# Optimization experiments

Measured on AMD Instinct MI355X. Metric: run time of the kernel, lower is better.

## Reference

```python
import jax, jax.numpy as jnp
import numpy as np

N, E, EMB, HID, FT, H = 2000, 32000, 768, 384, 768, 4
NEG_SLOPE = 0.2


def gat_conv(x, src, dst, edge_attr, W, a_src, a_dst, W_e, a_e, b):
    """PyG GATConv, concat=False (mean over heads), edge_dim, add_self_loops
    with fill_value='mean'. x:[N,Fin], edge_attr:[E,768]."""
    n = x.shape[0]
    h, c = a_src.shape
    # self loops: edge_attr of loop (i,i) = mean of incoming edge_attr at i
    deg = jax.ops.segment_sum(jnp.ones(src.shape[0], x.dtype), dst, num_segments=n)
    loop_attr = jax.ops.segment_sum(edge_attr, dst, num_segments=n) / jnp.maximum(deg, 1.0)[:, None]
    ar = jnp.arange(n)
    s = jnp.concatenate([src, ar])
    d = jnp.concatenate([dst, ar])
    ea = jnp.concatenate([edge_attr, loop_attr], axis=0)   # [E+N, 768]
    hx = (x @ W).reshape(n, h, c)                           # [N,H,C]
    he = (ea @ W_e).reshape(-1, h, c)                       # [E+N,H,C]
    alpha = (jnp.einsum('nhc,hc->nh', hx, a_src)[s]
             + jnp.einsum('nhc,hc->nh', hx, a_dst)[d]
             + jnp.einsum('ehc,hc->eh', he, a_e))           # [E+N,H]
    alpha = jax.nn.leaky_relu(alpha, NEG_SLOPE)
    # segment softmax over destination node (self loop guarantees nonempty)
    mx = jax.ops.segment_max(alpha, d, num_segments=n)
    ex = jnp.exp(alpha - mx[d])
    den = jax.ops.segment_sum(ex, d, num_segments=n)
    att = ex / den[d]                                       # [E+N,H]
    out = jax.ops.segment_sum(hx[s] * att[:, :, None], d, num_segments=n)  # [N,H,C]
    return out.mean(axis=1) + b


def setup_inputs() -> dict:
    key = jax.random.key(0)
    ks = jax.random.split(key, 16)
    w = lambda k, shape, s=0.05: (jax.random.normal(k, shape, jnp.float32) * s)
    return {
        'x': jax.random.randint(ks[0], (N, 2), 0, 178),
        'edge_index': jax.random.randint(ks[1], (2, E), 0, N),
        'edge_attr': jax.random.randint(ks[2], (E, 2), 0, 18),
        'x_emb': w(ks[3], (178, EMB)),
        'e_emb': w(ks[4], (18, EMB)),
        'W1': w(ks[5], (EMB, H * HID)),
        'as1': w(ks[6], (H, HID)),
        'ad1': w(ks[7], (H, HID)),
        'We1': w(ks[8], (EMB, H * HID)),
        'ae1': w(ks[9], (H, HID)),
        'b1': jnp.zeros((HID,), jnp.float32),
        'W2': w(ks[10], (HID, H * FT)),
        'as2': w(ks[11], (H, FT)),
        'ad2': w(ks[12], (H, FT)),
        'We2': w(ks[13], (EMB, H * FT)),
        'ae2': w(ks[14], (H, FT)),
        'b2': jnp.zeros((FT,), jnp.float32),
    }


def reference(x, edge_index, edge_attr, x_emb, e_emb, W1, as1, ad1, We1, ae1, b1,
              W2, as2, ad2, We2, ae2, b2):
    src, dst = edge_index[0], edge_index[1]
    xf = x_emb[x].sum(axis=1)          # [N,768]
    eaf = e_emb[edge_attr].sum(axis=1)  # [E,768]
    h = jax.nn.relu(gat_conv(xf, src, dst, eaf, W1, as1, ad1, We1, ae1, b1))
    out = gat_conv(h, src, dst, eaf, W2, as2, ad2, We2, ae2, b2)
    return out
```

## Files before the change

### kernel.cpp

```cpp
#include <hip/hip_runtime.h>
#include <hip/hip_bf16.h>

#define NN   2000
#define NE   32000
#define EMBD 768
#define NH   4
#define HID  384
#define NEG  0.2f
#define DCAP 128

#define GM 2000
#define GN 768
#define GK 1536
#define K1 768

typedef __bf16 bf16x8 __attribute__((ext_vector_type(8)));
typedef float  f32x4  __attribute__((ext_vector_type(4)));

__device__ inline float wsum(float v){
#pragma unroll
  for (int o = 32; o > 0; o >>= 1) v += __shfl_xor(v, o, 64);
  return v;
}
__device__ inline float wmax(float v){
#pragma unroll
  for (int o = 32; o > 0; o >>= 1) v = fmaxf(v, __shfl_xor(v, o, 64));
  return v;
}

__device__ inline unsigned short f2bf(float f){
  unsigned u = __float_as_uint(f);
  unsigned r = (u + 0x7FFFu + ((u >> 16) & 1u)) >> 16;
  return (unsigned short)r;
}
__device__ inline float bf2f(unsigned short h){
  return __uint_as_float(((unsigned)h) << 16);
}

__device__ inline void gload16(const void* g, void* l){
  __builtin_amdgcn_global_load_lds((const __attribute__((address_space(1))) void*)g,
                                   (__attribute__((address_space(3))) void*)l, 16, 0, 0);
}
__device__ inline float dot4(float4 a, float4 b){
  return a.x*b.x + a.y*b.y + a.z*b.z + a.w*b.w;
}

__global__ __launch_bounds__(1024) void k_cnt(const int* __restrict__ dst,
                                              int* __restrict__ offsets,
                                              int* __restrict__ cursor){
  __shared__ int cnt[NN];
  __shared__ int s[1024];
  int t = threadIdx.x;
  for (int i = t; i < NN; i += 1024) cnt[i] = 0;
  __syncthreads();
  for (int e = t; e < NE; e += 1024) atomicAdd(&cnt[dst[e]], 1);
  __syncthreads();
  int a = (2*t   < NN) ? cnt[2*t  ] : 0;
  int b = (2*t+1 < NN) ? cnt[2*t+1] : 0;
  s[t] = a + b;
  __syncthreads();
  for (int off = 1; off < 1024; off <<= 1){
    int v = (t >= off) ? s[t-off] : 0;
    __syncthreads();
    s[t] += v;
    __syncthreads();
  }
  int base = (t > 0) ? s[t-1] : 0;
  if (2*t < NN){ offsets[2*t] = base; cursor[2*t] = base; }
  if (2*t+1 < NN){ offsets[2*t+1] = base + a; cursor[2*t+1] = base + a; }
  if (2*t == NN) offsets[NN] = base;
}

__global__ void k_fill(const int* __restrict__ dst, int* __restrict__ cursor,
                       int* __restrict__ csr){
  int e = blockIdx.x * blockDim.x + threadIdx.x;
  if (e < NE){
    int p = atomicAdd(&cursor[dst[e]], 1);
    csr[p] = e;
  }
}

__global__ __launch_bounds__(256) void k_prep1(
    const float* __restrict__ We1, const float* __restrict__ ae1,
    const float* __restrict__ W2,  const float* __restrict__ as2,
    const float* __restrict__ ad2, const float* __restrict__ We2,
    const float* __restrict__ ae2,
    float* __restrict__ we_a1, float* __restrict__ wa_s2,
    float* __restrict__ wa_d2, float* __restrict__ we_a2){
  int wid = blockIdx.x*4 + (threadIdx.x >> 6);
  int lane = threadIdx.x & 63;
  bool lo32 = lane < 32;
  if (wid < 384){
    int kg = wid >> 2, h = wid & 3;
    int k0 = kg*8;
    const float4* ap = (const float4*)(ae1 + h*384);
    float4 a0 = ap[lane];
    float4 a1 = lo32 ? ap[64+lane] : make_float4(0,0,0,0);
    float res[8];
#pragma unroll
    for (int r = 0; r < 8; ++r){
      const float4* wr = (const float4*)(We1 + (size_t)(k0+r)*1536 + h*384);
      float s = dot4(wr[lane], a0);
      if (lo32) s += dot4(wr[64+lane], a1);
      res[r] = s;
    }
#pragma unroll
    for (int r = 0; r < 8; ++r) res[r] = wsum(res[r]);
    if (lane == 0){
#pragma unroll
      for (int r = 0; r < 8; ++r) we_a1[(k0+r)*4+h] = res[r];
    }
  } else if (wid < 768){
    int t2 = wid - 384;
    int kg = t2 >> 2, h = t2 & 3;
    int k0 = kg*4;
    const float4* s4 = (const float4*)(as2 + h*768);
    const float4* d4 = (const float4*)(ad2 + h*768);
    float4 sa[3], da[3];
#pragma unroll
    for (int i = 0; i < 3; ++i){ sa[i] = s4[i*64+lane]; da[i] = d4[i*64+lane]; }
    float r1[4], r2[4];
#pragma unroll
    for (int r = 0; r < 4; ++r){
      const float4* wr = (const float4*)(W2 + (size_t)(k0+r)*3072 + h*768);
      float s1 = 0.f, s2 = 0.f;
#pragma unroll
      for (int i = 0; i < 3; ++i){
        float4 w = wr[i*64+lane];
        s1 += dot4(w, sa[i]); s2 += dot4(w, da[i]);
      }
      r1[r] = s1; r2[r] = s2;
    }
#pragma unroll
    for (int r = 0; r < 4; ++r){ r1[r] = wsum(r1[r]); r2[r] = wsum(r2[r]); }
    if (lane == 0){
#pragma unroll
      for (int r = 0; r < 4; ++r){ wa_s2[(k0+r)*4+h] = r1[r]; wa_d2[(k0+r)*4+h] = r2[r]; }
    }
  } else {
    int t2 = wid - 768;
    int kg = t2 >> 2, h = t2 & 3;
    int k0 = kg*4;
    const float4* ap = (const float4*)(ae2 + h*768);
    float4 aa[3];
#pragma unroll
    for (int i = 0; i < 3; ++i) aa[i] = ap[i*64+lane];
    float res[4];
#pragma unroll
    for (int r = 0; r < 4; ++r){
      const float4* wr = (const float4*)(We2 + (size_t)(k0+r)*3072 + h*768);
      float s = 0.f;
#pragma unroll
      for (int i = 0; i < 3; ++i) s += dot4(wr[i*64+lane], aa[i]);
      res[r] = s;
    }
#pragma unroll
    for (int r = 0; r < 4; ++r) res[r] = wsum(res[r]);
    if (lane == 0){
#pragma unroll
      for (int r = 0; r < 4; ++r) we_a2[(k0+r)*4+h] = res[r];
    }
  }
}

__global__ __launch_bounds__(256) void k_bt(const float* __restrict__ W2,
                                            unsigned short* __restrict__ Bh,
                                            unsigned short* __restrict__ Bl){
  __shared__ float tile[64][65];
  int bk = blockIdx.x * 64;
  int bc = blockIdx.y * 64;
  int t = threadIdx.x;
  int cc = t & 63, kk4 = t >> 6;
#pragma unroll
  for (int i = 0; i < 16; ++i){
    int kk = kk4*16 + i;
    int k = bk + kk;
    int h = k / 384, kp = k - h*384;
    tile[kk][cc] = W2[(size_t)kp*3072 + h*768 + bc + cc];
  }
  __syncthreads();
  int kk2 = t & 63, cc4 = t >> 6;
#pragma unroll
  for (int i = 0; i < 16; ++i){
    int c2 = cc4*16 + i;
    float v = tile[kk2][c2];
    unsigned short hi = f2bf(v);
    unsigned short lo = f2bf(v - bf2f(hi));
    size_t o = (size_t)(bc + c2)*GK + bk + kk2;
    Bh[o] = hi; Bl[o] = lo;
  }
}

__global__ __launch_bounds__(256) void k_gemm1(const float* __restrict__ A,
                                               const float* __restrict__ B,
                                               float* __restrict__ P){
  __shared__ float As[16][34];
  __shared__ float Bs[16][68];
  int t = threadIdx.x;
  int bn = blockIdx.x * 64;
  int bm = blockIdx.y * 32;
  int s  = blockIdx.z;
  float acc[2][4] = {};
  int tm = t >> 4, tn = t & 15;
  int ar = t >> 3, ac = (t & 7) * 2;
  int br = t >> 4, bc = (t & 15) * 4;
  int kend = s*384 + 384;
  for (int k0 = s*384; k0 < kend; k0 += 16){
    float a0 = 0.f, a1 = 0.f;
    if (bm + ar < 178){
      const float* ap = &A[(size_t)(bm+ar)*EMBD + k0 + ac];
      a0 = ap[0]; a1 = ap[1];
    }
    As[ac][ar] = a0; As[ac+1][ar] = a1;
    *(float4*)&Bs[br][bc] = *(const float4*)&B[(size_t)(k0+br)*1536 + bn + bc];
    __syncthreads();
#pragma unroll
    for (int k = 0; k < 16; ++k){
      float x0 = As[k][tm*2], x1 = As[k][tm*2+1];
      float4 b4 = *(const float4*)&Bs[k][tn*4];
      acc[0][0] += x0*b4.x; acc[0][1] += x0*b4.y; acc[0][2] += x0*b4.z; acc[0][3] += x0*b4.w;
      acc[1][0] += x1*b4.x; acc[1][1] += x1*b4.y; acc[1][2] += x1*b4.z; acc[1][3] += x1*b4.w;
    }
    __syncthreads();
  }
#pragma unroll
  for (int i = 0; i < 2; ++i){
    int r = bm + tm*2 + i;
    if (r < 178){
      float4 v; v.x=acc[i][0]; v.y=acc[i][1]; v.z=acc[i][2]; v.w=acc[i][3];
      *(float4*)&P[(size_t)s*178*1536 + (size_t)r*1536 + bn + tn*4] = v;
    }
  }
}

__global__ __launch_bounds__(256) void k_prepB(
    const float* __restrict__ parts,
    const float* __restrict__ as1, const float* __restrict__ ad1,
    const float* __restrict__ e_emb,
    const float* __restrict__ we_a1, const float* __restrict__ we_a2,
    unsigned short* __restrict__ XHh, unsigned short* __restrict__ XHl,
    float* __restrict__ xa_s1, float* __restrict__ xa_d1,
    float* __restrict__ ew1, float* __restrict__ ew2){
  int blk = blockIdx.x, t = threadIdx.x;
  if (blk < 178){
    int tok = blk;
    for (int i = t; i < 1536; i += 256){
      float v = parts[(size_t)tok*1536 + i] + parts[(size_t)(178+tok)*1536 + i];
      int h = i / 384, c = i - h*384;
      size_t off = (size_t)c*K1 + h*192 + tok;
      unsigned short hi = f2bf(v);
      XHh[off] = hi; XHl[off] = f2bf(v - bf2f(hi));
    }
  } else if (blk < 356){
    int r = blk - 178;
    int h = t >> 6, lane = t & 63;
    const float4* p0 = (const float4*)(parts + (size_t)r*1536 + h*384);
    const float4* p1 = (const float4*)(parts + (size_t)(178 + r)*1536 + h*384);
    const float4* s4 = (const float4*)(as1 + h*384);
    const float4* d4 = (const float4*)(ad1 + h*384);
    float s1, s2;
    {
      float4 a = p0[lane], b = p1[lane], sa = s4[lane], da = d4[lane];
      float4 u; u.x=a.x+b.x; u.y=a.y+b.y; u.z=a.z+b.z; u.w=a.w+b.w;
      s1 = u.x*sa.x + u.y*sa.y + u.z*sa.z + u.w*sa.w;
      s2 = u.x*da.x + u.y*da.y + u.z*da.z + u.w*da.w;
    }
    if (lane < 32){
      float4 a = p0[64+lane], b = p1[64+lane], sa = s4[64+lane], da = d4[64+lane];
      float4 u; u.x=a.x+b.x; u.y=a.y+b.y; u.z=a.z+b.z; u.w=a.w+b.w;
      s1 += u.x*sa.x + u.y*sa.y + u.z*sa.z + u.w*sa.w;
      s2 += u.x*da.x + u.y*da.y + u.z*da.z + u.w*da.w;
    }
    s1 = wsum(s1); s2 = wsum(s2);
    if (lane == 0){ xa_s1[r*4+h] = s1; xa_d1[r*4+h] = s2; }
  } else if (blk < 392){
    int id = (blk - 356)*4 + (t >> 6);
    int lane = t & 63;
    const float* wv = (id < 72) ? we_a1 : we_a2;
    float* o = (id < 72) ? ew1 : ew2;
    int id2 = (id < 72) ? id : (id - 72);
    int r = id2 >> 2, h = id2 & 3;
    const float* ar = e_emb + (size_t)r*EMBD;
    float acc = 0.f;
    for (int k = lane; k < EMBD; k += 64) acc += ar[k] * wv[k*4+h];
    acc = wsum(acc);
    if (lane == 0) o[r*4+h] = acc;
  } else {
    int i = (blk - 392)*256 + t;
    if (i < 21504){
      int c = i / 56, rem = i - c*56;
      int h = rem / 14, tp = 178 + rem - h*14;
      size_t off = (size_t)c*K1 + h*192 + tp;
      XHh[off] = 0; XHl[off] = 0;
    }
  }
}

__global__ __launch_bounds__(256) void k_gat1sm(const int* __restrict__ offsets,
                      int* __restrict__ csr, const int* __restrict__ srcv,
                      const int* __restrict__ x, const int* __restrict__ ea,
                      const float* __restrict__ xa_s1, const float* __restrict__ xa_d1,
                      const float* __restrict__ ew1, float* __restrict__ spill,
                      unsigned short* __restrict__ Qh, unsigned short* __restrict__ Ql){
  __shared__ float wts[DCAP][5];
  __shared__ int   sE[DCAP];
  __shared__ int   sA[DCAP], sB[DCAP];
  __shared__ float coef[K1];
  int n = blockIdx.x, t = threadIdx.x;
  int w = t >> 6, lane = t & 63;
  int lo = offsets[n], hi = offsets[n+1];
  int deg = hi - lo;
  bool big = deg > DCAP;

  if (!big){
    int m = 1; while (m < deg) m <<= 1;
    for (int i = t; i < m; i += 256) sE[i] = (i < deg) ? csr[lo+i] : 0x7fffffff;
    __syncthreads();
    for (int k = 2; k <= m; k <<= 1){
      for (int j2 = k >> 1; j2 > 0; j2 >>= 1){
        for (int i = t; i < m; i += 256){
          int ixj = i ^ j2;
          if (ixj > i){
            int a = sE[i], b = sE[ixj];
            bool up = ((i & k) == 0);
            if ((a > b) == up){ sE[i] = b; sE[ixj] = a; }
          }
        }
        __syncthreads();
      }
    }
    for (int i = t; i < deg; i += 256) csr[lo+i] = sE[i];
  } else {
    if (t == 0){
      for (int i = lo+1; i < hi; ++i){
        int v = csr[i], j = i-1;
        while (j >= lo && csr[j] > v){ csr[j+1] = csr[j]; --j; }
        csr[j+1] = v;
      }
    }
  }
  for (int i = t; i < K1; i += 256) coef[i] = 0.f;
  __syncthreads();

  int xn0 = x[2*n], xn1 = x[2*n+1];
  float ad_n = xa_d1[xn0*4+w] + xa_d1[xn1*4+w];
  float as_n = xa_s1[xn0*4+w] + xa_s1[xn1*4+w];
  float mx = -3.4e38f, sae = 0.f;
  float wlv;
  if (!big){
    for (int j = lane; j < deg; j += 64){
      int e = sE[j]; int s = srcv[e];
      int a = x[2*s], b = x[2*s+1];
      if (w == 0){ sA[j] = a; sB[j] = b; }
      float ae = ew1[ea[2*e]*4+w] + ew1[ea[2*e+1]*4+w];
      float al = (xa_s1[a*4+w] + xa_s1[b*4+w]) + ad_n + ae;
      al = (al > 0.f) ? al : NEG * al;
      wts[j][w] = al;
      sae += ae; mx = fmaxf(mx, al);
    }
    mx = wmax(mx); sae = wsum(sae);
    float all_ = as_n + ad_n + sae / fmaxf((float)deg, 1.f);
    all_ = (all_ > 0.f) ? all_ : NEG * all_;
    mx = fmaxf(mx, all_);
    float den = 0.f;
    for (int j = lane; j < deg; j += 64){
      float xx = expf(wts[j][w] - mx);
      wts[j][w] = xx; den += xx;
    }
    den = wsum(den);
    float exl = expf(all_ - mx);
    den += exl;
    float inv = 1.f / den;
    for (int j = lane; j < deg; j += 64) wts[j][w] *= inv;
    wlv = exl * inv;
  } else {
    for (int p = lo + lane; p < hi; p += 64){
      int e = csr[p]; int s = srcv[e];
      int a = x[2*s], b = x[2*s+1];
      float ae = ew1[ea[2*e]*4+w] + ew1[ea[2*e+1]*4+w];
      float al = (xa_s1[a*4+w] + xa_s1[b*4+w]) + ad_n + ae;
      al = (al > 0.f) ? al : NEG * al;
      spill[e*4 + w] = al;
      sae += ae; mx = fmaxf(mx, al);
    }
    mx = wmax(mx); sae = wsum(sae);
    float all_ = as_n + ad_n + sae / fmaxf((float)deg, 1.f);
    all_ = (all_ > 0.f) ? all_ : NEG * all_;
    mx = fmaxf(mx, all_);
    float den = 0.f;
    for (int p = lo + lane; p < hi; p += 64){
      int e = csr[p];
      float xx = expf(spill[e*4 + w] - mx);
      spill[e*4 + w] = xx; den += xx;
    }
    den = wsum(den);
    float exl = expf(all_ - mx);
    den += exl;
    float inv = 1.f / den;
    for (int p = lo + lane; p < hi; p += 64) spill[csr[p]*4 + w] *= inv;
    wlv = exl * inv;
  }
  __syncthreads();

  if (lane == 0){
    float* cf = coef + w*192;
    if (!big){
      for (int j = 0; j < deg; ++j){
        float wj = wts[j][w];
        cf[sA[j]] += wj; cf[sB[j]] += wj;
      }
    } else {
      for (int p = lo; p < hi; ++p){
        int e = csr[p]; int s = srcv[e];
        float wj = spill[e*4 + w];
        cf[x[2*s]] += wj; cf[x[2*s+1]] += wj;
      }
    }
    cf[xn0] += wlv; cf[xn1] += wlv;
  }
  __syncthreads();

  for (int i = t; i < K1; i += 256){
    float v = coef[i];
    unsigned short hi16 = f2bf(v);
    Qh[(size_t)n*K1 + i] = hi16;
    Ql[(size_t)n*K1 + i] = f2bf(v - bf2f(hi16));
  }
}

__global__ __launch_bounds__(256) void k_mm1(const unsigned short* __restrict__ Qh,
                                             const unsigned short* __restrict__ Ql,
                                             const unsigned short* __restrict__ XHh,
                                             const unsigned short* __restrict__ XHl,
                                             const float* __restrict__ b1,
                                             float* __restrict__ hact){
  __shared__ __align__(16) unsigned short lds[2][4][64][64];
  int b = blockIdx.x;
  int xcd = b & 7, idx = b >> 3;
  int bm = xcd*4 + idx/6, bn = idx % 6;
  int wave = threadIdx.x >> 6, lane = threadIdx.x & 63;
  int wm = wave >> 1, wn = wave & 1;
  int rl = lane & 15, kq = lane >> 4;

  int rt   = lane >> 3;
  int kswz = ((lane & 7) ^ rt) * 8;
  const unsigned short* sbase;
  int rowbase;
  if (wave == 0){ sbase = Qh; rowbase = bm*64; }
  else if (wave == 1){ sbase = Ql; rowbase = bm*64; }
  else if (wave == 2){ sbase = XHh; rowbase = bn*64; }
  else { sbase = XHl; rowbase = bn*64; }
  bool isA = wave < 2;

  f32x4 acc[2][2] = {};

#pragma unroll
  for (int i = 0; i < 8; ++i){
    int row = rowbase + i*8 + rt;
    if (isA) row = (row < GM) ? row : (GM-1);
    gload16(sbase + (size_t)row*K1 + kswz, &lds[0][wave][i*8][0]);
  }
  __syncthreads();

  for (int t = 0; t < 12; ++t){
    int cur = t & 1;
    if (t < 11){
      int k0 = (t+1)*64;
#pragma unroll
      for (int i = 0; i < 8; ++i){
        int row = rowbase + i*8 + rt;
        if (isA) row = (row < GM) ? row : (GM-1);
        gload16(sbase + (size_t)row*K1 + k0 + kswz, &lds[cur^1][wave][i*8][0]);
      }
    }
#pragma unroll
    for (int ks = 0; ks < 2; ++ks){
      bf16x8 ah[2], al2[2], bh2[2], bl2[2];
#pragma unroll
      for (int i = 0; i < 2; ++i){
        int r = wm*32 + i*16 + rl;
        int sl = (ks*4 + kq) ^ (r & 7);
        ah[i]  = *(const bf16x8*)&lds[cur][0][r][sl*8];
        al2[i] = *(const bf16x8*)&lds[cur][1][r][sl*8];
      }
#pragma unroll
      for (int j = 0; j < 2; ++j){
        int cdx = wn*32 + j*16 + rl;
        int sl = (ks*4 + kq) ^ (cdx & 7);
        bh2[j] = *(const bf16x8*)&lds[cur][2][cdx][sl*8];
        bl2[j] = *(const bf16x8*)&lds[cur][3][cdx][sl*8];
      }
#pragma unroll
      for (int i = 0; i < 2; ++i){
#pragma unroll
        for (int j = 0; j < 2; ++j){
          acc[i][j] = __builtin_amdgcn_mfma_f32_16x16x32_bf16(ah[i],  bh2[j], acc[i][j], 0, 0, 0);
          acc[i][j] = __builtin_amdgcn_mfma_f32_16x16x32_bf16(ah[i],  bl2[j], acc[i][j], 0, 0, 0);
          acc[i][j] = __builtin_amdgcn_mfma_f32_16x16x32_bf16(al2[i], bh2[j], acc[i][j], 0, 0, 0);
        }
      }
    }
    __syncthreads();
  }

#pragma unroll
  for (int i = 0; i < 2; ++i){
#pragma unroll
    for (int j = 0; j < 2; ++j){
      int col = bn*64 + wn*32 + j*16 + rl;
      float bb = b1[col];
#pragma unroll
      for (int r = 0; r < 4; ++r){
        int row = bm*64 + wm*32 + i*16 + kq*4 + r;
        if (row < GM) hact[(size_t)row*HID + col] = fmaxf(0.25f*acc[i][j][r] + bb, 0.f);
      }
    }
  }
}

__global__ __launch_bounds__(256) void k_dots(const float* __restrict__ hact,
                      const float* __restrict__ wa_s2, const float* __restrict__ wa_d2,
                      float* __restrict__ asrc2, float* __restrict__ adst2){
  int w = threadIdx.x >> 6, lane = threadIdx.x & 63;
  int n = blockIdx.x*4 + w;
  float pr[8] = {};
#pragma unroll
  for (int i = 0; i < 6; ++i){
    int c = i*64 + lane;
    float v = hact[(size_t)n*HID + c];
#pragma unroll
    for (int h = 0; h < 4; ++h){
      pr[h]   += v * wa_s2[c*4+h];
      pr[4+h] += v * wa_d2[c*4+h];
    }
  }
#pragma unroll
  for (int o = 32; o > 0; o >>= 1){
#pragma unroll
    for (int q = 0; q < 8; ++q) pr[q] += __shfl_xor(pr[q], o, 64);
  }
  if (lane == 0){
#pragma unroll
    for (int h = 0; h < 4; ++h){ asrc2[n*4+h] = pr[h]; adst2[n*4+h] = pr[4+h]; }
  }
}

__global__ __launch_bounds__(384) void k_gat2(const int* __restrict__ offsets,
                      const int* __restrict__ csr, const int* __restrict__ srcv,
                      const int* __restrict__ ea,
                      const float* __restrict__ asrc, const float* __restrict__ adst,
                      const float* __restrict__ ew2,
                      const float* __restrict__ hact, float* __restrict__ spill,
                      unsigned short* __restrict__ Gh, unsigned short* __restrict__ Gl){
  __shared__ float wts[DCAP][5];
  __shared__ int   ssrc[DCAP];
  __shared__ float wl[4];
  int n = blockIdx.x, t = threadIdx.x;
  int w = t >> 6, lane = t & 63;
  int lo = offsets[n], hi = offsets[n+1];
  int deg = hi - lo;
  bool big = deg > DCAP;
  if (w < 4){
    float ad_n = adst[n*NH + w];
    float as_n = asrc[n*NH + w];
    float mx = -3.4e38f, sae = 0.f;
    if (!big){
      for (int p = lo + lane; p < hi; p += 64){
        int e = csr[p]; int s = srcv[e];
        if (w == 0) ssrc[p - lo] = s;
        float ae = ew2[ea[2*e]*4+w] + ew2[ea[2*e+1]*4+w];
        float al = asrc[s*NH + w] + ad_n + ae;
        al = (al > 0.f) ? al : NEG * al;
        wts[p - lo][w] = al;
        sae += ae; mx = fmaxf(mx, al);
      }
      mx = wmax(mx); sae = wsum(sae);
      float all_ = as_n + ad_n + sae / fmaxf((float)deg, 1.f);
      all_ = (all_ > 0.f) ? all_ : NEG * all_;
      mx = fmaxf(mx, all_);
      float den = 0.f;
      for (int p = lo + lane; p < hi; p += 64){
        float xx = expf(wts[p - lo][w] - mx);
        wts[p - lo][w] = xx; den += xx;
      }
      den = wsum(den);
      float exl = expf(all_ - mx);
      den += exl;
      float inv = 1.f / den;
      for (int p = lo + lane; p < hi; p += 64) wts[p - lo][w] *= inv;
      if (lane == 0) wl[w] = exl * inv;
    } else {
      for (int p = lo + lane; p < hi; p += 64){
        int e = csr[p];
        float ae = ew2[ea[2*e]*4+w] + ew2[ea[2*e+1]*4+w];
        float al = asrc[srcv[e]*NH + w] + ad_n + ae;
        al = (al > 0.f) ? al : NEG * al;
        spill[e*4 + w] = al;
        sae += ae; mx = fmaxf(mx, al);
      }
      mx = wmax(mx); sae = wsum(sae);
      float all_ = as_n + ad_n + sae / fmaxf((float)deg, 1.f);
      all_ = (all_ > 0.f) ? all_ : NEG * all_;
      mx = fmaxf(mx, all_);
      float den = 0.f;
      for (int p = lo + lane; p < hi; p += 64){
        int e = csr[p];
        float xx = expf(spill[e*4 + w] - mx);
        spill[e*4 + w] = xx; den += xx;
      }
      den = wsum(den);
      float exl = expf(all_ - mx);
      den += exl;
      float inv = 1.f / den;
      for (int p = lo + lane; p < hi; p += 64) spill[csr[p]*4 + w] *= inv;
      if (lane == 0) wl[w] = exl * inv;
    }
  }
  __syncthreads();

  int c = t;
  float a0 = 0.f, a1 = 0.f, a2 = 0.f, a3 = 0.f;
  if (!big){
    float vnext = 0.f;
    if (deg > 0) vnext = hact[(size_t)ssrc[0]*HID + c];
    for (int j = 0; j < deg; ++j){
      float vc = vnext;
      if (j+1 < deg) vnext = hact[(size_t)ssrc[j+1]*HID + c];
      float w0=wts[j][0], w1=wts[j][1], w2=wts[j][2], w3=wts[j][3];
      a0 += w0*vc; a1 += w1*vc; a2 += w2*vc; a3 += w3*vc;
    }
  } else {
    for (int j = 0; j < deg; ++j){
      int e = csr[lo+j]; int s = srcv[e];
      float w0 = spill[e*4+0], w1 = spill[e*4+1], w2 = spill[e*4+2], w3 = spill[e*4+3];
      float vc = hact[(size_t)s*HID + c];
      a0 += w0*vc; a1 += w1*vc; a2 += w2*vc; a3 += w3*vc;
    }
  }
  {
    float vc = hact[(size_t)n*HID + c];
    a0 += wl[0]*vc; a1 += wl[1]*vc; a2 += wl[2]*vc; a3 += wl[3]*vc;
  }
  size_t base = (size_t)n*GK + c;
  float vv[4] = {a0, a1, a2, a3};
#pragma unroll
  for (int h = 0; h < 4; ++h){
    unsigned short hi16 = f2bf(vv[h]);
    unsigned short lo16 = f2bf(vv[h] - bf2f(hi16));
    Gh[base + h*384] = hi16;
    Gl[base + h*384] = lo16;
  }
}

__global__ __launch_bounds__(256) void k_mm2(const unsigned short* __restrict__ Gh,
                                             const unsigned short* __restrict__ Gl,
                                             const unsigned short* __restrict__ Bh,
                                             const unsigned short* __restrict__ Bl,
                                             const float* __restrict__ b2,
                                             float* __restrict__ out){
  __shared__ __align__(16) unsigned short lds[2][4][64][64];
  int b = blockIdx.x;
  int xcd = b & 7, idx = b >> 3;
  int bm = xcd*4 + idx/12, bn = idx % 12;
  int wave = threadIdx.x >> 6, lane = threadIdx.x & 63;
  int wm = wave >> 1, wn = wave & 1;
  int rl = lane & 15, kq = lane >> 4;

  int rt   = lane >> 3;
  int kswz = ((lane & 7) ^ rt) * 8;
  const unsigned short* sbase;
  int rowbase;
  if (wave == 0){ sbase = Gh; rowbase = bm*64; }
  else if (wave == 1){ sbase = Gl; rowbase = bm*64; }
  else if (wave == 2){ sbase = Bh; rowbase = bn*64; }
  else { sbase = Bl; rowbase = bn*64; }
  bool isA = wave < 2;

  f32x4 acc[2][2] = {};

#pragma unroll
  for (int i = 0; i < 8; ++i){
    int row = rowbase + i*8 + rt;
    if (isA) row = (row < GM) ? row : (GM-1);
    gload16(sbase + (size_t)row*GK + kswz, &lds[0][wave][i*8][0]);
  }
  __syncthreads();

  for (int t = 0; t < 24; ++t){
    int cur = t & 1;
    if (t < 23){
      int k0 = (t+1)*64;
#pragma unroll
      for (int i = 0; i < 8; ++i){
        int row = rowbase + i*8 + rt;
        if (isA) row = (row < GM) ? row : (GM-1);
        gload16(sbase + (size_t)row*GK + k0 + kswz, &lds[cur^1][wave][i*8][0]);
      }
    }
#pragma unroll
    for (int ks = 0; ks < 2; ++ks){
      bf16x8 ah[2], al2[2], bh2[2], bl2[2];
#pragma unroll
      for (int i = 0; i < 2; ++i){
        int r = wm*32 + i*16 + rl;
        int sl = (ks*4 + kq) ^ (r & 7);
        ah[i]  = *(const bf16x8*)&lds[cur][0][r][sl*8];
        al2[i] = *(const bf16x8*)&lds[cur][1][r][sl*8];
      }
#pragma unroll
      for (int j = 0; j < 2; ++j){
        int cdx = wn*32 + j*16 + rl;
        int sl = (ks*4 + kq) ^ (cdx & 7);
        bh2[j] = *(const bf16x8*)&lds[cur][2][cdx][sl*8];
        bl2[j] = *(const bf16x8*)&lds[cur][3][cdx][sl*8];
      }
#pragma unroll
      for (int i = 0; i < 2; ++i){
#pragma unroll
        for (int j = 0; j < 2; ++j){
          acc[i][j] = __builtin_amdgcn_mfma_f32_16x16x32_bf16(ah[i],  bh2[j], acc[i][j], 0, 0, 0);
          acc[i][j] = __builtin_amdgcn_mfma_f32_16x16x32_bf16(ah[i],  bl2[j], acc[i][j], 0, 0, 0);
          acc[i][j] = __builtin_amdgcn_mfma_f32_16x16x32_bf16(al2[i], bh2[j], acc[i][j], 0, 0, 0);
        }
      }
    }
    __syncthreads();
  }

#pragma unroll
  for (int i = 0; i < 2; ++i){
#pragma unroll
    for (int j = 0; j < 2; ++j){
      int col = bn*64 + wn*32 + j*16 + rl;
      float bb = b2[col];
#pragma unroll
      for (int r = 0; r < 4; ++r){
        int row = bm*64 + wm*32 + i*16 + kq*4 + r;
        if (row < GM) out[(size_t)row*GN + col] = 0.25f*acc[i][j][r] + bb;
      }
    }
  }
}

extern "C" void kernel_launch(void* const* d_in, const int* in_sizes, int n_in,
                              void* d_out, int out_size, void* d_ws, size_t ws_size,
                              hipStream_t stream){
  const int*   x     = (const int*)d_in[0];
  const int*   ei    = (const int*)d_in[1];
  const int*   ea    = (const int*)d_in[2];
  const float* x_emb = (const float*)d_in[3];
  const float* e_emb = (const float*)d_in[4];
  const float* W1    = (const float*)d_in[5];
  const float* as1   = (const float*)d_in[6];
  const float* ad1   = (const float*)d_in[7];
  const float* We1   = (const float*)d_in[8];
  const float* ae1   = (const float*)d_in[9];
  const float* b1    = (const float*)d_in[10];
  const float* W2    = (const float*)d_in[11];
  const float* as2   = (const float*)d_in[12];
  const float* ad2   = (const float*)d_in[13];
  const float* We2   = (const float*)d_in[14];
  const float* ae2   = (const float*)d_in[15];
  const float* b2    = (const float*)d_in[16];
  const int* srcv = ei;
  const int* dstv = ei + NE;
  float* out = (float*)d_out;

  char* p = (char*)d_ws;
  auto take = [&](size_t n){ void* q = (void*)p; p += (n + 255) & ~(size_t)255; return q; };
  int*   cursor  = (int*)take(NN*4);
  int*   offsets = (int*)take((NN+1)*4);
  int*   csr     = (int*)take(NE*4);
  float* we_a1   = (float*)take(EMBD*NH*4);
  float* wa_s2   = (float*)take(HID*NH*4);
  float* wa_d2   = (float*)take(HID*NH*4);
  float* we_a2   = (float*)take(EMBD*NH*4);
  float* xa_s1   = (float*)take(178*NH*4);
  float* xa_d1   = (float*)take(178*NH*4);
  float* ew1     = (float*)take(18*NH*4);
  float* ew2     = (float*)take(18*NH*4);
  float* parts1  = (float*)take((size_t)2*178*1536*4);
  unsigned short* XHh = (unsigned short*)take((size_t)HID*K1*2);
  unsigned short* XHl = (unsigned short*)take((size_t)HID*K1*2);
  unsigned short* Qh  = (unsigned short*)take((size_t)NN*K1*2);
  unsigned short* Ql  = (unsigned short*)take((size_t)NN*K1*2);
  unsigned short* Bth = (unsigned short*)take((size_t)GN*GK*2);
  unsigned short* Btl = (unsigned short*)take((size_t)GN*GK*2);
  unsigned short* Gh  = (unsigned short*)take((size_t)GM*GK*2);
  unsigned short* Gl  = (unsigned short*)take((size_t)GM*GK*2);
  float* spill   = (float*)take((size_t)NE*NH*4);
  float* hact    = (float*)take((size_t)NN*HID*4);
  float* asrc2   = (float*)take(NN*NH*4);
  float* adst2   = (float*)take(NN*NH*4);

  k_cnt<<<1, 1024, 0, stream>>>(dstv, offsets, cursor);
  k_fill<<<(NE+255)/256, 256, 0, stream>>>(dstv, cursor, csr);

  k_prep1<<<384, 256, 0, stream>>>(We1, ae1, W2, as2, ad2, We2, ae2,
                                   we_a1, wa_s2, wa_d2, we_a2);
  { dim3 g(GK/64, GN/64); k_bt<<<g, 256, 0, stream>>>(W2, Bth, Btl); }
  { dim3 g(24, 6, 2); k_gemm1<<<g, 256, 0, stream>>>(x_emb, W1, parts1); }
  k_prepB<<<476, 256, 0, stream>>>(parts1, as1, ad1, e_emb, we_a1, we_a2,
                                   XHh, XHl, xa_s1, xa_d1, ew1, ew2);

  k_gat1sm<<<NN, 256, 0, stream>>>(offsets, csr, srcv, x, ea, xa_s1, xa_d1,
                                   ew1, spill, Qh, Ql);
  k_mm1<<<192, 256, 0, stream>>>(Qh, Ql, XHh, XHl, b1, hact);
  k_dots<<<500, 256, 0, stream>>>(hact, wa_s2, wa_d2, asrc2, adst2);

  k_gat2<<<NN, 384, 0, stream>>>(offsets, csr, srcv, ea, asrc2, adst2, ew2,
                                 hact, spill, Gh, Gl);

  k_mm2<<<384, 256, 0, stream>>>(Gh, Gl, Bth, Btl, b2, out);
}
```

Before: 133.1 us.

## Replace FP32 SIMT embedding GEMM with split-bf16 MFMA GEMM

The x_emb @ W1 product (178x768x1536) moves from a split-K FP32 SIMT kernel to a bf16x3 (hi/lo split) MFMA kernel with a double-buffered swizzled LDS pipeline. A merged transpose/convert kernel now also produces the transposed hi/lo W1 and hi/lo x_emb alongside the W2 transpose, so the split-K partial sum buffer and its reduction in k_prepB go away. The cost is extra conversion traffic for W1 (about 1.2M elements) and only 72 blocks in the new GEMM. Accuracy relies on the three-term bf16 split.

```diff
diff --git a/kernel.cpp b/kernel.cpp
--- a/kernel.cpp
+++ b/kernel.cpp
@@ -163,78 +163,163 @@
   }
 }
 
-__global__ __launch_bounds__(256) void k_bt(const float* __restrict__ W2,
+__global__ __launch_bounds__(256) void k_tr(const float* __restrict__ W2,
+                                            const float* __restrict__ W1,
+                                            const float* __restrict__ x_emb,
                                             unsigned short* __restrict__ Bh,
-                                            unsigned short* __restrict__ Bl){
+                                            unsigned short* __restrict__ Bl,
+                                            unsigned short* __restrict__ W1th,
+                                            unsigned short* __restrict__ W1tl,
+                                            unsigned short* __restrict__ Xeh,
+                                            unsigned short* __restrict__ Xel){
   __shared__ float tile[64][65];
-  int bk = blockIdx.x * 64;
-  int bc = blockIdx.y * 64;
-  int t = threadIdx.x;
-  int cc = t & 63, kk4 = t >> 6;
-#pragma unroll
-  for (int i = 0; i < 16; ++i){
-    int kk = kk4*16 + i;
-    int k = bk + kk;
-    int h = k / 384, kp = k - h*384;
-    tile[kk][cc] = W2[(size_t)kp*3072 + h*768 + bc + cc];
-  }
-  __syncthreads();
-  int kk2 = t & 63, cc4 = t >> 6;
-#pragma unroll
-  for (int i = 0; i < 16; ++i){
-    int c2 = cc4*16 + i;
-    float v = tile[kk2][c2];
-    unsigned short hi = f2bf(v);
-    unsigned short lo = f2bf(v - bf2f(hi));
-    size_t o = (size_t)(bc + c2)*GK + bk + kk2;
-    Bh[o] = hi; Bl[o] = lo;
-  }
-}
-
-__global__ __launch_bounds__(256) void k_gemm1(const float* __restrict__ A,
-                                               const float* __restrict__ B,
-                                               float* __restrict__ P){
-  __shared__ float As[16][34];
-  __shared__ float Bs[16][68];
-  int t = threadIdx.x;
-  int bn = blockIdx.x * 64;
-  int bm = blockIdx.y * 32;
-  int s  = blockIdx.z;
-  float acc[2][4] = {};
-  int tm = t >> 4, tn = t & 15;
-  int ar = t >> 3, ac = (t & 7) * 2;
-  int br = t >> 4, bc = (t & 15) * 4;
-  int kend = s*384 + 384;
-  for (int k0 = s*384; k0 < kend; k0 += 16){
-    float a0 = 0.f, a1 = 0.f;
-    if (bm + ar < 178){
-      const float* ap = &A[(size_t)(bm+ar)*EMBD + k0 + ac];
-      a0 = ap[0]; a1 = ap[1];
-    }
-    As[ac][ar] = a0; As[ac+1][ar] = a1;
-    *(float4*)&Bs[br][bc] = *(const float4*)&B[(size_t)(k0+br)*1536 + bn + bc];
+  int blk = blockIdx.x, t = threadIdx.x;
+  if (blk < 288){
+    int bk = (blk % 24) * 64;
+    int bc = (blk / 24) * 64;
+    int cc = t & 63, kk4 = t >> 6;
+#pragma unroll
+    for (int i = 0; i < 16; ++i){
+      int kk = kk4*16 + i;
+      int k = bk + kk;
+      int h = k / 384, kp = k - h*384;
+      tile[kk][cc] = W2[(size_t)kp*3072 + h*768 + bc + cc];
+    }
     __syncthreads();
-#pragma unroll
-    for (int k = 0; k < 16; ++k){
-      float x0 = As[k][tm*2], x1 = As[k][tm*2+1];
-      float4 b4 = *(const float4*)&Bs[k][tn*4];
-      acc[0][0] += x0*b4.x; acc[0][1] += x0*b4.y; acc[0][2] += x0*b4.z; acc[0][3] += x0*b4.w;
-      acc[1][0] += x1*b4.x; acc[1][1] += x1*b4.y; acc[1][2] += x1*b4.z; acc[1][3] += x1*b4.w;
+    int kk2 = t & 63, cc4 = t >> 6;
+#pragma unroll
+    for (int i = 0; i < 16; ++i){
+      int c2 = cc4*16 + i;
+      float v = tile[kk2][c2];
+      unsigned short hi = f2bf(v);
+      unsigned short lo = f2bf(v - bf2f(hi));
+      size_t o = (size_t)(bc + c2)*GK + bk + kk2;
+      Bh[o] = hi; Bl[o] = lo;
+    }
+  } else if (blk < 576){
+    int idx = blk - 288;
+    int bkk = (idx % 12) * 64;
+    int bcc = (idx / 12) * 64;
+    int cc = t & 63, kk4 = t >> 6;
+#pragma unroll
+    for (int i = 0; i < 16; ++i){
+      int kk = kk4*16 + i;
+      tile[kk][cc] = W1[(size_t)(bkk+kk)*1536 + bcc + cc];
     }
     __syncthreads();
-  }
+    int kk2 = t & 63, cc4 = t >> 6;
+#pragma unroll
+    for (int i = 0; i < 16; ++i){
+      int c2 = cc4*16 + i;
+      float v = tile[kk2][c2];
+      unsigned short hi = f2bf(v);
+      unsigned short lo = f2bf(v - bf2f(hi));
+      size_t o = (size_t)(bcc + c2)*768 + bkk + kk2;
+      W1th[o] = hi; W1tl[o] = lo;
+    }
+  } else {
+    int i = (blk - 576)*256 + t;
+    if (i < 34176){
+      float4 v = ((const float4*)x_emb)[i];
+      unsigned short h0 = f2bf(v.x), h1 = f2bf(v.y), h2 = f2bf(v.z), h3 = f2bf(v.w);
+      ushort4 hh; hh.x = h0; hh.y = h1; hh.z = h2; hh.w = h3;
+      ushort4 ll; ll.x = f2bf(v.x - bf2f(h0)); ll.y = f2bf(v.y - bf2f(h1));
+      ll.z = f2bf(v.z - bf2f(h2)); ll.w = f2bf(v.w - bf2f(h3));
+      ((ushort4*)Xeh)[i] = hh;
+      ((ushort4*)Xel)[i] = ll;
+    }
+  }
+}
+
+__global__ __launch_bounds__(256) void k_mmX(const unsigned short* __restrict__ Ah,
+                                             const unsigned short* __restrict__ Al,
+                                             const unsigned short* __restrict__ Bh,
+                                             const unsigned short* __restrict__ Bl,
+                                             float* __restrict__ xh1){
+  __shared__ __align__(16) unsigned short lds[2][4][64][64];
+  int b = blockIdx.x;
+  int bm = b / 24, bn = b % 24;
+  int wave = threadIdx.x >> 6, lane = threadIdx.x & 63;
+  int wm = wave >> 1, wn = wave & 1;
+  int rl = lane & 15, kq = lane >> 4;
+
+  int rt   = lane >> 3;
+  int kswz = ((lane & 7) ^ rt) * 8;
+  const unsigned short* sbase;
+  int rowbase;
+  if (wave == 0){ sbase = Ah; rowbase = bm*64; }
+  else if (wave == 1){ sbase = Al; rowbase = bm*64; }
+  else if (wave == 2){ sbase = Bh; rowbase = bn*64; }
+  else { sbase = Bl; rowbase = bn*64; }
+  bool isA = wave < 2;
+
+  f32x4 acc[2][2] = {};
+
+#pragma unroll
+  for (int i = 0; i < 8; ++i){
+    int row = rowbase + i*8 + rt;
+    if (isA) row = (row < 178) ? row : 177;
+    gload16(sbase + (size_t)row*768 + kswz, &lds[0][wave][i*8][0]);
+  }
+  __syncthreads();
+
+  for (int t = 0; t < 12; ++t){
+    int cur = t & 1;
+    if (t < 11){
+      int k0 = (t+1)*64;
+#pragma unroll
+      for (int i = 0; i < 8; ++i){
+        int row = rowbase + i*8 + rt;
+        if (isA) row = (row < 178) ? row : 177;
+        gload16(sbase + (size_t)row*768 + k0 + kswz, &lds[cur^1][wave][i*8][0]);
+      }
+    }
+#pragma unroll
+    for (int ks = 0; ks < 2; ++ks){
+      bf16x8 ah[2], al2[2], bh2[2], bl2[2];
+#pragma unroll
+      for (int i = 0; i < 2; ++i){
+        int r = wm*32 + i*16 + rl;
+        int sl = (ks*4 + kq) ^ (r & 7);
+        ah[i]  = *(const bf16x8*)&lds[cur][0][r][sl*8];
+        al2[i] = *(const bf16x8*)&lds[cur][1][r][sl*8];
+      }
+#pragma unroll
+      for (int j = 0; j < 2; ++j){
+        int cdx = wn*32 + j*16 + rl;
+        int sl = (ks*4 + kq) ^ (cdx & 7);
+        bh2[j] = *(const bf16x8*)&lds[cur][2][cdx][sl*8];
+        bl2[j] = *(const bf16x8*)&lds[cur][3][cdx][sl*8];
+      }
+#pragma unroll
+      for (int i = 0; i < 2; ++i){
+#pragma unroll
+        for (int j = 0; j < 2; ++j){
+          acc[i][j] = __builtin_amdgcn_mfma_f32_16x16x32_bf16(ah[i],  bh2[j], acc[i][j], 0, 0, 0);
+          acc[i][j] = __builtin_amdgcn_mfma_f32_16x16x32_bf16(ah[i],  bl2[j], acc[i][j], 0, 0, 0);
+          acc[i][j] = __builtin_amdgcn_mfma_f32_16x16x32_bf16(al2[i], bh2[j], acc[i][j], 0, 0, 0);
+        }
+      }
+    }
+    __syncthreads();
+  }
+
 #pragma unroll
   for (int i = 0; i < 2; ++i){
-    int r = bm + tm*2 + i;
-    if (r < 178){
-      float4 v; v.x=acc[i][0]; v.y=acc[i][1]; v.z=acc[i][2]; v.w=acc[i][3];
-      *(float4*)&P[(size_t)s*178*1536 + (size_t)r*1536 + bn + tn*4] = v;
+#pragma unroll
+    for (int j = 0; j < 2; ++j){
+      int col = bn*64 + wn*32 + j*16 + rl;
+#pragma unroll
+      for (int r = 0; r < 4; ++r){
+        int row = bm*64 + wm*32 + i*16 + kq*4 + r;
+        if (row < 178) xh1[(size_t)row*1536 + col] = acc[i][j][r];
+      }
     }
   }
 }
 
 __global__ __launch_bounds__(256) void k_prepB(
-    const float* __restrict__ parts,
+    const float* __restrict__ xh1,
     const float* __restrict__ as1, const float* __restrict__ ad1,
     const float* __restrict__ e_emb,
     const float* __restrict__ we_a1, const float* __restrict__ we_a2,
@@ -245,7 +330,7 @@
   if (blk < 178){
     int tok = blk;
     for (int i = t; i < 1536; i += 256){
-      float v = parts[(size_t)tok*1536 + i] + parts[(size_t)(178+tok)*1536 + i];
+      float v = xh1[(size_t)tok*1536 + i];
       int h = i / 384, c = i - h*384;
       size_t off = (size_t)c*K1 + h*192 + tok;
       unsigned short hi = f2bf(v);
@@ -254,22 +339,17 @@
   } else if (blk < 356){
     int r = blk - 178;
     int h = t >> 6, lane = t & 63;
-    const float4* p0 = (const float4*)(parts + (size_t)r*1536 + h*384);
-    const float4* p1 = (const float4*)(parts + (size_t)(178 + r)*1536 + h*384);
+    const float4* p0 = (const float4*)(xh1 + (size_t)r*1536 + h*384);
     const float4* s4 = (const float4*)(as1 + h*384);
     const float4* d4 = (const float4*)(ad1 + h*384);
     float s1, s2;
     {
-      float4 a = p0[lane], b = p1[lane], sa = s4[lane], da = d4[lane];
-      float4 u; u.x=a.x+b.x; u.y=a.y+b.y; u.z=a.z+b.z; u.w=a.w+b.w;
-      s1 = u.x*sa.x + u.y*sa.y + u.z*sa.z + u.w*sa.w;
-      s2 = u.x*da.x + u.y*da.y + u.z*da.z + u.w*da.w;
+      float4 u = p0[lane], sa = s4[lane], da = d4[lane];
+      s1 = dot4(u, sa); s2 = dot4(u, da);
     }
     if (lane < 32){
-      float4 a = p0[64+lane], b = p1[64+lane], sa = s4[64+lane], da = d4[64+lane];
-      float4 u; u.x=a.x+b.x; u.y=a.y+b.y; u.z=a.z+b.z; u.w=a.w+b.w;
-      s1 += u.x*sa.x + u.y*sa.y + u.z*sa.z + u.w*sa.w;
-      s2 += u.x*da.x + u.y*da.y + u.z*da.z + u.w*da.w;
+      float4 u = p0[64+lane], sa = s4[64+lane], da = d4[64+lane];
+      s1 += dot4(u, sa); s2 += dot4(u, da);
     }
     s1 = wsum(s1); s2 = wsum(s2);
     if (lane == 0){ xa_s1[r*4+h] = s1; xa_d1[r*4+h] = s2; }
@@ -779,15 +859,19 @@
   float* xa_d1   = (float*)take(178*NH*4);
   float* ew1     = (float*)take(18*NH*4);
   float* ew2     = (float*)take(18*NH*4);
-  float* parts1  = (float*)take((size_t)2*178*1536*4);
-  unsigned short* XHh = (unsigned short*)take((size_t)HID*K1*2);
-  unsigned short* XHl = (unsigned short*)take((size_t)HID*K1*2);
-  unsigned short* Qh  = (unsigned short*)take((size_t)NN*K1*2);
-  unsigned short* Ql  = (unsigned short*)take((size_t)NN*K1*2);
-  unsigned short* Bth = (unsigned short*)take((size_t)GN*GK*2);
-  unsigned short* Btl = (unsigned short*)take((size_t)GN*GK*2);
-  unsigned short* Gh  = (unsigned short*)take((size_t)GM*GK*2);
-  unsigned short* Gl  = (unsigned short*)take((size_t)GM*GK*2);
+  float* xh1     = (float*)take((size_t)178*1536*4);
+  unsigned short* Xeh  = (unsigned short*)take((size_t)178*768*2);
+  unsigned short* Xel  = (unsigned short*)take((size_t)178*768*2);
+  unsigned short* W1th = (unsigned short*)take((size_t)1536*768*2);
+  unsigned short* W1tl = (unsigned short*)take((size_t)1536*768*2);
+  unsigned short* XHh  = (unsigned short*)take((size_t)HID*K1*2);
+  unsigned short* XHl  = (unsigned short*)take((size_t)HID*K1*2);
+  unsigned short* Qh   = (unsigned short*)take((size_t)NN*K1*2);
+  unsigned short* Ql   = (unsigned short*)take((size_t)NN*K1*2);
+  unsigned short* Bth  = (unsigned short*)take((size_t)GN*GK*2);
+  unsigned short* Btl  = (unsigned short*)take((size_t)GN*GK*2);
+  unsigned short* Gh   = (unsigned short*)take((size_t)GM*GK*2);
+  unsigned short* Gl   = (unsigned short*)take((size_t)GM*GK*2);
   float* spill   = (float*)take((size_t)NE*NH*4);
   float* hact    = (float*)take((size_t)NN*HID*4);
   float* asrc2   = (float*)take(NN*NH*4);
@@ -798,9 +882,9 @@
 
   k_prep1<<<384, 256, 0, stream>>>(We1, ae1, W2, as2, ad2, We2, ae2,
                                    we_a1, wa_s2, wa_d2, we_a2);
-  { dim3 g(GK/64, GN/64); k_bt<<<g, 256, 0, stream>>>(W2, Bth, Btl); }
-  { dim3 g(24, 6, 2); k_gemm1<<<g, 256, 0, stream>>>(x_emb, W1, parts1); }
-  k_prepB<<<476, 256, 0, stream>>>(parts1, as1, ad1, e_emb, we_a1, we_a2,
+  k_tr<<<710, 256, 0, stream>>>(W2, W1, x_emb, Bth, Btl, W1th, W1tl, Xeh, Xel);
+  k_mmX<<<72, 256, 0, stream>>>(Xeh, Xel, W1th, W1tl, xh1);
+  k_prepB<<<476, 256, 0, stream>>>(xh1, as1, ad1, e_emb, we_a1, we_a2,
                                    XHh, XHl, xa_s1, xa_d1, ew1, ew2);
 
   k_gat1sm<<<NN, 256, 0, stream>>>(offsets, csr, srcv, x, ea, xa_s1, xa_d1,
```

Result: faster. 124.5 us (-6.5%).
